# Performance work log

Measured on AMD Instinct MI355X. Metric: run time of the kernel, lower is better.

The kernel has to match this reference:

```python
import jax, jax.numpy as jnp
import numpy as np

B, T, C = 8, 2048, 1024
HEAD = 64
BLOCK = 2048  # block_size == max_size == ramp_size


def setup_inputs() -> dict:
    key = jax.random.key(0)
    kx, kq, kk, kv = jax.random.split(key, 4)
    x = jax.random.normal(kx, (B, T, C), dtype=jnp.float32)
    # torch Linear(n_embd, head_size, bias=False): store as (C, HEAD) for x @ W
    s = 1.0 / np.sqrt(C)
    Wq = jax.random.uniform(kq, (C, HEAD), dtype=jnp.float32, minval=-s, maxval=s)
    Wk = jax.random.uniform(kk, (C, HEAD), dtype=jnp.float32, minval=-s, maxval=s)
    Wv = jax.random.uniform(kv, (C, HEAD), dtype=jnp.float32, minval=-s, maxval=s)
    # adaptive_span current_val parameter, shape (1,1,1), init 0
    current_val = jnp.zeros((1, 1, 1), dtype=jnp.float32)
    return {"x": x, "Wq": Wq, "Wk": Wk, "Wv": Wv, "current_val": current_val}


def reference(x, Wq, Wk, Wv, current_val):
    Bb, Tt, Cc = x.shape
    q = x @ Wq  # (B,T,H)
    k = x @ Wk
    v = x @ Wv
    scale = 1.0 / jnp.sqrt(jnp.asarray(HEAD, dtype=x.dtype))
    scores = jnp.einsum('bth,bsh->bts', q, k) * scale  # (B,T,T)
    causal = jnp.tril(jnp.ones((Tt, Tt), dtype=bool))
    scores = jnp.where(causal, scores, -jnp.inf)
    w = jax.nn.softmax(scores, axis=-1)
    # adaptive span post-softmax mask (T == max_size here, so no slicing)
    template = jnp.linspace(1.0 - BLOCK, 0.0, BLOCK, dtype=x.dtype)  # (T,)
    span = template + current_val * BLOCK  # (1,1,T)
    span = jnp.clip(span / BLOCK + 1.0, 0.0, 1.0)
    w = w * span
    w = w / (w.sum(-1, keepdims=True) + 1e-8)
    # dropout p=0 (eval) -> identity
    out = jnp.einsum('bts,bsh->bth', w, v)  # (B,T,H)
    return out
```

## Files before the change

kernel.cpp:

```cpp
#include <hip/hip_runtime.h>
#include <hip/hip_bf16.h>

#define BSZ 8
#define T 2048
#define C 1024
#define H 64
#define M (BSZ*T)

typedef __attribute__((ext_vector_type(4))) float f32x4;
typedef __attribute__((ext_vector_type(8))) short bf16x8;
typedef __attribute__((ext_vector_type(4))) short s16x4;
typedef __attribute__((ext_vector_type(8))) short s16x8;

static __device__ __forceinline__ short f2bf(float f) {
  union { float f; unsigned u; } c; c.f = f;
  unsigned u = c.u;
  u = (u + 0x7fffu + ((u >> 16) & 1u)) >> 16;
  return (short)u;
}

static __device__ __forceinline__ float fexp2(float x) {
  float r;
  asm("v_exp_f32 %0, %1" : "=v"(r) : "v"(x));
  return r;
}

__global__ __launch_bounds__(256) void k_wt(const float* __restrict__ Wq,
                                            const float* __restrict__ Wk,
                                            const float* __restrict__ Wv,
                                            short* __restrict__ wt) {
  int idx = blockIdx.x * 256 + threadIdx.x;
  int c = idx & (C - 1);
  int n = idx >> 10;
  int w = n >> 6;
  int h = n & (H - 1);
  const float* W = (w == 0) ? Wq : (w == 1) ? Wk : Wv;
  wt[idx] = f2bf(W[c * H + h]);
}

__global__ __launch_bounds__(256) void k_qkv(const float* __restrict__ x,
                                             const short* __restrict__ wt,
                                             short* __restrict__ qb,
                                             short* __restrict__ kb,
                                             short* __restrict__ vt) {
  __shared__ short xs[2][32 * 64];
  __shared__ short wl[2][192 * 64];
  const int tid = threadIdx.x;
  const int m0 = blockIdx.x * 32;
  const int lane = tid & 63;
  const int wid = tid >> 6;
  const int g16 = lane >> 4, l16 = lane & 15;
  const int row0 = (wid & 1) * 16;
  const int nc0 = (wid >> 1) * 96;

  f32x4 acc[6];
  #pragma unroll
  for (int i = 0; i < 6; ++i) acc[i] = (f32x4){0.f, 0.f, 0.f, 0.f};

  const int xr = tid >> 4;
  const int xc4 = (tid & 15) * 4;
  const int xsw = xc4 ^ ((xr & 7) << 3);
  const int wr = tid >> 3;
  const int wc8 = (tid & 7) * 8;
  const int wsw = wc8 ^ ((wr & 7) << 3);
  const int fsw = (l16 & 7) << 3;

  float4 xA0, xA1, xB0, xB1;
  s16x8 wA0, wA1, wA2, wA3, wA4, wA5;
  s16x8 wB0, wB1, wB2, wB3, wB4, wB5;

#define QKV_LOAD(S, kc) do { \
    x##S##0 = *(const float4*)&x[(size_t)(m0 + xr) * C + (kc) + xc4]; \
    x##S##1 = *(const float4*)&x[(size_t)(m0 + xr + 16) * C + (kc) + xc4]; \
    w##S##0 = *(const s16x8*)&wt[(wr +   0) * C + (kc) + wc8]; \
    w##S##1 = *(const s16x8*)&wt[(wr +  32) * C + (kc) + wc8]; \
    w##S##2 = *(const s16x8*)&wt[(wr +  64) * C + (kc) + wc8]; \
    w##S##3 = *(const s16x8*)&wt[(wr +  96) * C + (kc) + wc8]; \
    w##S##4 = *(const s16x8*)&wt[(wr + 128) * C + (kc) + wc8]; \
    w##S##5 = *(const s16x8*)&wt[(wr + 160) * C + (kc) + wc8]; \
  } while (0)

#define QKV_STORE(S, buf) do { \
    s16x4 h0 = { f2bf((x##S##0).x), f2bf((x##S##0).y), f2bf((x##S##0).z), f2bf((x##S##0).w) }; \
    s16x4 h1 = { f2bf((x##S##1).x), f2bf((x##S##1).y), f2bf((x##S##1).z), f2bf((x##S##1).w) }; \
    *(s16x4*)&xs[buf][xr * 64 + xsw] = h0; \
    *(s16x4*)&xs[buf][(xr + 16) * 64 + xsw] = h1; \
    *(s16x8*)&wl[buf][(wr +   0) * 64 + wsw] = w##S##0; \
    *(s16x8*)&wl[buf][(wr +  32) * 64 + wsw] = w##S##1; \
    *(s16x8*)&wl[buf][(wr +  64) * 64 + wsw] = w##S##2; \
    *(s16x8*)&wl[buf][(wr +  96) * 64 + wsw] = w##S##3; \
    *(s16x8*)&wl[buf][(wr + 128) * 64 + wsw] = w##S##4; \
    *(s16x8*)&wl[buf][(wr + 160) * 64 + wsw] = w##S##5; \
  } while (0)

#define QKV_COMPUTE(buf) do { \
    _Pragma("unroll") \
    for (int ks = 0; ks < 2; ++ks) { \
      bf16x8 a = *(const bf16x8*)&xs[buf][(row0 + l16) * 64 + ((ks * 32 + g16 * 8) ^ fsw)]; \
      _Pragma("unroll") \
      for (int nt = 0; nt < 6; ++nt) { \
        bf16x8 bfr = *(const bf16x8*)&wl[buf][(nc0 + nt * 16 + l16) * 64 + ((ks * 32 + g16 * 8) ^ fsw)]; \
        acc[nt] = __builtin_amdgcn_mfma_f32_16x16x32_bf16(a, bfr, acc[nt], 0, 0, 0); \
      } \
    } \
  } while (0)

  QKV_LOAD(A, 0);
  QKV_STORE(A, 0);
  QKV_LOAD(B, 64);
  __syncthreads();

  #pragma unroll 1
  for (int ii = 0; ii < 8; ++ii) {
    if (ii < 7) QKV_LOAD(A, (2 * ii + 2) * 64);
    QKV_STORE(B, 1);
    QKV_COMPUTE(0);
    __syncthreads();
    if (ii < 7) {
      QKV_LOAD(B, (2 * ii + 3) * 64);
      QKV_STORE(A, 0);
    }
    QKV_COMPUTE(1);
    if (ii < 7) __syncthreads();
  }
#undef QKV_LOAD
#undef QKV_STORE
#undef QKV_COMPUTE

  const int r0 = row0 + g16 * 4;
  #pragma unroll
  for (int nt = 0; nt < 6; ++nt) {
    const int nglob = nc0 + nt * 16;
    const int which = nglob >> 6;
    const int col = (nglob & 63) + l16;
    #pragma unroll
    for (int j = 0; j < 4; ++j) {
      const int tg = m0 + r0 + j;
      const short val = f2bf(acc[nt][j]);
      if (which == 0)      qb[tg * H + col] = val;
      else if (which == 1) kb[tg * H + col] = val;
      else {
        const int b = tg >> 11, tl = tg & (T - 1);
        vt[((b << 6) + col) * T + tl] = val;
      }
    }
  }
}

__global__ __launch_bounds__(512, 2) void k_attn(const short* __restrict__ qb,
                                                 const short* __restrict__ kb,
                                                 const short* __restrict__ vt,
                                                 const float* __restrict__ cvp,
                                                 float* __restrict__ out) {
  __shared__ float Ow[8][16][68];
  __shared__ float mw[8][16];
  __shared__ float Lw[8][16];
  const int pid = blockIdx.x;
  const int b = pid & 7;
  const int pr = pid >> 3;
  const int q0A = pr << 4, q0B = (127 - pr) << 4;
  const int nitA = (q0A + 47) >> 5;
  const int nitB = (q0B + 47) >> 5;
  const int NT = nitA + nitB;
  int wA = (8 * nitA + (NT >> 1)) / NT;
  wA = wA < 1 ? 1 : (wA > 7 ? 7 : wA);

  const int tid = threadIdx.x;
  const int wid = tid >> 6;
  const int lane = tid & 63;
  const int g16 = lane >> 4, l16 = lane & 15;
  const float cv = cvp[0];
  const float SCL = 0.125f * 1.44269504f;

  const bool onA = (wid < wA);
  const int q0 = onA ? q0A : q0B;
  const int nitW = onA ? nitA : nitB;
  const int nwt = onA ? wA : 8 - wA;
  const int wg = onA ? wid : wid - wA;
  const int npw = (nitW + nwt - 1) / nwt;
  const int lo = wg * npw;
  const int hi = (lo + npw < nitW) ? lo + npw : nitW;

  const short* qp = qb + ((size_t)(b << 11) + q0 + l16) * H + g16 * 8;
  bf16x8 qf0 = *(const bf16x8*)qp;
  bf16x8 qf1 = *(const bf16x8*)(qp + 32);
  const int qg = q0 + l16;

  const int gsel = (g16 & 1) << 5;
  const int addrA = (gsel + l16) << 2;
  const int addrB = (gsel + 16 + l16) << 2;
  const bool ghi = (g16 >= 2);

  float m = -3e38f, L = 0.f;
  f32x4 O[4];
  #pragma unroll
  for (int t4 = 0; t4 < 4; ++t4) O[t4] = (f32x4){0.f, 0.f, 0.f, 0.f};

  if (lo < hi) {
    const short* kp = kb + ((size_t)(b << 11) + lo * 32 + l16) * H + g16 * 8;
    const short* vp = vt + ((size_t)(b << 6) + l16) * T + lo * 32 + g16 * 8;
    bf16x8 k00 = *(const bf16x8*)kp;
    bf16x8 k01 = *(const bf16x8*)(kp + 32);
    bf16x8 k02 = *(const bf16x8*)(kp + 16 * H);
    bf16x8 k03 = *(const bf16x8*)(kp + 16 * H + 32);
    kp += 32 * H;
    bf16x8 k10 = k00, k11 = k01, k12 = k02, k13 = k03;
    if (lo + 1 < hi) {
      k10 = *(const bf16x8*)kp;
      k11 = *(const bf16x8*)(kp + 32);
      k12 = *(const bf16x8*)(kp + 16 * H);
      k13 = *(const bf16x8*)(kp + 16 * H + 32);
      kp += 32 * H;
    }

    #pragma unroll 1
    for (int it = lo; it < hi; it += 2) {
      const bool has2 = (it + 1 < hi);
      bf16x8 vA0 = *(const bf16x8*)vp;
      bf16x8 vA1 = *(const bf16x8*)(vp + 16 * T);
      bf16x8 vA2 = *(const bf16x8*)(vp + 32 * T);
      bf16x8 vA3 = *(const bf16x8*)(vp + 48 * T);
      bf16x8 vB0 = vA0, vB1 = vA1, vB2 = vA2, vB3 = vA3;
      if (has2) {
        vB0 = *(const bf16x8*)(vp + 32);
        vB1 = *(const bf16x8*)(vp + 16 * T + 32);
        vB2 = *(const bf16x8*)(vp + 32 * T + 32);
        vB3 = *(const bf16x8*)(vp + 48 * T + 32);
      }
      bf16x8 n00, n01, n02, n03, n10, n11, n12, n13;
      const bool pf0 = (it + 2 < hi), pf1 = (it + 3 < hi);
      if (pf0) {
        n00 = *(const bf16x8*)kp;
        n01 = *(const bf16x8*)(kp + 32);
        n02 = *(const bf16x8*)(kp + 16 * H);
        n03 = *(const bf16x8*)(kp + 16 * H + 32);
        kp += 32 * H;
      }
      if (pf1) {
        n10 = *(const bf16x8*)kp;
        n11 = *(const bf16x8*)(kp + 32);
        n12 = *(const bf16x8*)(kp + 16 * H);
        n13 = *(const bf16x8*)(kp + 16 * H + 32);
        kp += 32 * H;
      }

      f32x4 sA0 = {0.f,0.f,0.f,0.f}, sA1 = {0.f,0.f,0.f,0.f};
      f32x4 sB0 = {0.f,0.f,0.f,0.f}, sB1 = {0.f,0.f,0.f,0.f};
      sA0 = __builtin_amdgcn_mfma_f32_16x16x32_bf16(k00, qf0, sA0, 0, 0, 0);
      sB0 = __builtin_amdgcn_mfma_f32_16x16x32_bf16(k10, qf0, sB0, 0, 0, 0);
      sA1 = __builtin_amdgcn_mfma_f32_16x16x32_bf16(k02, qf0, sA1, 0, 0, 0);
      sB1 = __builtin_amdgcn_mfma_f32_16x16x32_bf16(k12, qf0, sB1, 0, 0, 0);
      sA0 = __builtin_amdgcn_mfma_f32_16x16x32_bf16(k01, qf1, sA0, 0, 0, 0);
      sB0 = __builtin_amdgcn_mfma_f32_16x16x32_bf16(k11, qf1, sB0, 0, 0, 0);
      sA1 = __builtin_amdgcn_mfma_f32_16x16x32_bf16(k03, qf1, sA1, 0, 0, 0);
      sB1 = __builtin_amdgcn_mfma_f32_16x16x32_bf16(k13, qf1, sB1, 0, 0, 0);

      const int kv0A = it << 5, kv0B = kv0A + 32;
      const int kvbA = kv0A + g16 * 4, kvbB = kv0B + g16 * 4;
      const bool diagA = (kv0A + 31 > q0);
      float svA[8], svB[8];
      if (diagA) {
        #pragma unroll
        for (int r = 0; r < 8; ++r) {
          const int kvg = kvbA + ((r >> 2) << 4) + (r & 3);
          const float s = ((r < 4) ? sA0[r] : sA1[r - 4]) * SCL;
          svA[r] = (kvg <= qg) ? s : -1e30f;
        }
      } else {
        #pragma unroll
        for (int r = 0; r < 8; ++r)
          svA[r] = ((r < 4) ? sA0[r] : sA1[r - 4]) * SCL;
      }
      if (has2) {
        const bool diagB = (kv0B + 31 > q0);
        if (diagB) {
          #pragma unroll
          for (int r = 0; r < 8; ++r) {
            const int kvg = kvbB + ((r >> 2) << 4) + (r & 3);
            const float s = ((r < 4) ? sB0[r] : sB1[r - 4]) * SCL;
            svB[r] = (kvg <= qg) ? s : -1e30f;
          }
        } else {
          #pragma unroll
          for (int r = 0; r < 8; ++r)
            svB[r] = ((r < 4) ? sB0[r] : sB1[r - 4]) * SCL;
        }
      } else {
        #pragma unroll
        for (int r = 0; r < 8; ++r) svB[r] = -1e30f;
      }

      float pmax = -3e38f;
      #pragma unroll
      for (int r = 0; r < 8; ++r) pmax = fmaxf(pmax, fmaxf(svA[r], svB[r]));
      if (!__all(pmax <= m + 7.f)) {
        float v = pmax;
        v = fmaxf(v, __shfl_xor(v, 16, 64));
        v = fmaxf(v, __shfl_xor(v, 32, 64));
        const float mn = fmaxf(m, v);
        const float al = fexp2(m - mn);
        m = mn;
        L *= al;
        #pragma unroll
        for (int t4 = 0; t4 < 4; ++t4) O[t4] *= al;
      }

      float pA[8], pB[8];
      #pragma unroll
      for (int r = 0; r < 8; ++r) {
        const int kvgA = kvbA + ((r >> 2) << 4) + (r & 3);
        const float spA = fminf(fmaxf((float)(kvgA + 1) * (1.f / 2048.f) + cv, 0.f), 1.f);
        pA[r] = fexp2(svA[r] - m) * spA;
        const float spB = fminf(fmaxf((float)(kvgA + 33) * (1.f / 2048.f) + cv, 0.f), 1.f);
        pB[r] = fexp2(svB[r] - m) * spB;
      }
      if (diagA) {
        #pragma unroll
        for (int r = 0; r < 8; ++r) {
          const int kvg = kvbA + ((r >> 2) << 4) + (r & 3);
          pA[r] = (kvg <= qg) ? pA[r] : 0.f;
          pB[r] = (kvg + 32 <= qg) ? pB[r] : 0.f;
        }
      } else if (kv0B + 31 > q0) {
        #pragma unroll
        for (int r = 0; r < 8; ++r) {
          const int kvg = kvbB + ((r >> 2) << 4) + (r & 3);
          pB[r] = (kvg <= qg) ? pB[r] : 0.f;
        }
      }
      L += ((pA[0] + pA[1]) + (pA[2] + pA[3])) + ((pA[4] + pA[5]) + (pA[6] + pA[7]))
         + ((pB[0] + pB[1]) + (pB[2] + pB[3])) + ((pB[4] + pB[5]) + (pB[6] + pB[7]));

      union { float f; unsigned u; } a0, a1;
      unsigned dA0, dA1, dA2, dA3, dB0, dB1, dB2, dB3;
      a0.f = pA[0]; a1.f = pA[1]; dA0 = (a0.u >> 16) | (a1.u & 0xffff0000u);
      a0.f = pA[2]; a1.f = pA[3]; dA1 = (a0.u >> 16) | (a1.u & 0xffff0000u);
      a0.f = pA[4]; a1.f = pA[5]; dA2 = (a0.u >> 16) | (a1.u & 0xffff0000u);
      a0.f = pA[6]; a1.f = pA[7]; dA3 = (a0.u >> 16) | (a1.u & 0xffff0000u);
      a0.f = pB[0]; a1.f = pB[1]; dB0 = (a0.u >> 16) | (a1.u & 0xffff0000u);
      a0.f = pB[2]; a1.f = pB[3]; dB1 = (a0.u >> 16) | (a1.u & 0xffff0000u);
      a0.f = pB[4]; a1.f = pB[5]; dB2 = (a0.u >> 16) | (a1.u & 0xffff0000u);
      a0.f = pB[6]; a1.f = pB[7]; dB3 = (a0.u >> 16) | (a1.u & 0xffff0000u);
      const int Alo0 = __builtin_amdgcn_ds_bpermute(addrA, (int)dA0);
      const int Alo1 = __builtin_amdgcn_ds_bpermute(addrA, (int)dA1);
      const int Alo2 = __builtin_amdgcn_ds_bpermute(addrB, (int)dA0);
      const int Alo3 = __builtin_amdgcn_ds_bpermute(addrB, (int)dA1);
      const int Ahi0 = __builtin_amdgcn_ds_bpermute(addrA, (int)dA2);
      const int Ahi1 = __builtin_amdgcn_ds_bpermute(addrA, (int)dA3);
      const int Ahi2 = __builtin_amdgcn_ds_bpermute(addrB, (int)dA2);
      const int Ahi3 = __builtin_amdgcn_ds_bpermute(addrB, (int)dA3);
      const int Blo0 = __builtin_amdgcn_ds_bpermute(addrA, (int)dB0);
      const int Blo1 = __builtin_amdgcn_ds_bpermute(addrA, (int)dB1);
      const int Blo2 = __builtin_amdgcn_ds_bpermute(addrB, (int)dB0);
      const int Blo3 = __builtin_amdgcn_ds_bpermute(addrB, (int)dB1);
      const int Bhi0 = __builtin_amdgcn_ds_bpermute(addrA, (int)dB2);
      const int Bhi1 = __builtin_amdgcn_ds_bpermute(addrA, (int)dB3);
      const int Bhi2 = __builtin_amdgcn_ds_bpermute(addrB, (int)dB2);
      const int Bhi3 = __builtin_amdgcn_ds_bpermute(addrB, (int)dB3);
      union { int w[4]; bf16x8 v8; } puA, puB;
      puA.w[0] = ghi ? Ahi0 : Alo0;
      puA.w[1] = ghi ? Ahi1 : Alo1;
      puA.w[2] = ghi ? Ahi2 : Alo2;
      puA.w[3] = ghi ? Ahi3 : Alo3;
      puB.w[0] = ghi ? Bhi0 : Blo0;
      puB.w[1] = ghi ? Bhi1 : Blo1;
      puB.w[2] = ghi ? Bhi2 : Blo2;
      puB.w[3] = ghi ? Bhi3 : Blo3;
      const bf16x8 paA = puA.v8;
      const bf16x8 paB = puB.v8;

      O[0] = __builtin_amdgcn_mfma_f32_16x16x32_bf16(vA0, paA, O[0], 0, 0, 0);
      O[1] = __builtin_amdgcn_mfma_f32_16x16x32_bf16(vA1, paA, O[1], 0, 0, 0);
      O[2] = __builtin_amdgcn_mfma_f32_16x16x32_bf16(vA2, paA, O[2], 0, 0, 0);
      O[3] = __builtin_amdgcn_mfma_f32_16x16x32_bf16(vA3, paA, O[3], 0, 0, 0);
      if (has2) {
        O[0] = __builtin_amdgcn_mfma_f32_16x16x32_bf16(vB0, paB, O[0], 0, 0, 0);
        O[1] = __builtin_amdgcn_mfma_f32_16x16x32_bf16(vB1, paB, O[1], 0, 0, 0);
        O[2] = __builtin_amdgcn_mfma_f32_16x16x32_bf16(vB2, paB, O[2], 0, 0, 0);
        O[3] = __builtin_amdgcn_mfma_f32_16x16x32_bf16(vB3, paB, O[3], 0, 0, 0);
      }

      if (pf0) { k00 = n00; k01 = n01; k02 = n02; k03 = n03; }
      if (pf1) { k10 = n10; k11 = n11; k12 = n12; k13 = n13; }
      vp += 64;
    }
  }

  float Lr = L;
  Lr += __shfl_xor(Lr, 16, 64);
  Lr += __shfl_xor(Lr, 32, 64);
  if (g16 == 0) { mw[wid][l16] = m; Lw[wid][l16] = Lr; }
  #pragma unroll
  for (int t4 = 0; t4 < 4; ++t4)
    *(f32x4*)&Ow[wid][l16][t4 * 16 + g16 * 4] = O[t4];
  __syncthreads();

  {
    const int r32 = tid >> 4;
    const int c4 = (tid & 15) << 2;
    const bool rowA = (r32 < 16);
    const int r = rowA ? r32 : r32 - 16;
    const int w0 = rowA ? 0 : wA;
    const int w1 = rowA ? wA : 8;
    const int q0r = rowA ? q0A : q0B;
    float Mx = -3e38f;
    for (int w = w0; w < w1; ++w) Mx = fmaxf(Mx, mw[w][r]);
    float Ls = 0.f;
    f32x4 o = (f32x4){0.f, 0.f, 0.f, 0.f};
    for (int w = w0; w < w1; ++w) {
      const float fw = fexp2(mw[w][r] - Mx);
      Ls += Lw[w][r] * fw;
      f32x4 ow = *(const f32x4*)&Ow[w][r][c4];
      o += ow * fw;
    }
    o *= 1.f / (Ls + 1e-30f);
    *(f32x4*)&out[(size_t)((b << 11) + q0r + r) * H + c4] = o;
  }
}

extern "C" void kernel_launch(void* const* d_in, const int* in_sizes, int n_in,
                              void* d_out, int out_size, void* d_ws, size_t ws_size,
                              hipStream_t stream) {
  const float* x  = (const float*)d_in[0];
  const float* Wq = (const float*)d_in[1];
  const float* Wk = (const float*)d_in[2];
  const float* Wv = (const float*)d_in[3];
  const float* cv = (const float*)d_in[4];
  float* out = (float*)d_out;

  char* ws = (char*)d_ws;
  short* qb = (short*)(ws);
  short* kb = (short*)(ws + (size_t)M * H * 2);
  short* vt = (short*)(ws + (size_t)2 * M * H * 2);
  short* wt = (short*)(ws + (size_t)3 * M * H * 2);

  hipLaunchKernelGGL(k_wt, dim3(3 * H * C / 256), dim3(256), 0, stream, Wq, Wk, Wv, wt);
  hipLaunchKernelGGL(k_qkv, dim3(M / 32), dim3(256), 0, stream, x, wt, qb, kb, vt);
  hipLaunchKernelGGL(k_attn, dim3(BSZ * T / 32), dim3(512), 0, stream, qb, kb, vt, cv, out);
}
```

Measured before the change: 66.31 us.

## Load QKV projection MFMA fragments directly from global, dropping LDS staging

The QKV projection kernel no longer stages x and the weights through shared memory with barriers. Each wave now loads its own MFMA operand fragments straight from global memory into registers, converts x to bf16 on the fly, and software-pipelines the loads against the MFMAs. This removes LDS traffic and __syncthreads, and launch bounds now request two blocks per CU. The cost is redundant global loads across waves, which must be absorbed by the cache, plus more register pressure.

```diff
diff --git a/kernel.cpp b/kernel.cpp
--- a/kernel.cpp
+++ b/kernel.cpp
@@ -38,13 +38,11 @@
   wt[idx] = f2bf(W[c * H + h]);
 }
 
-__global__ __launch_bounds__(256) void k_qkv(const float* __restrict__ x,
-                                             const short* __restrict__ wt,
-                                             short* __restrict__ qb,
-                                             short* __restrict__ kb,
-                                             short* __restrict__ vt) {
-  __shared__ short xs[2][32 * 64];
-  __shared__ short wl[2][192 * 64];
+__global__ __launch_bounds__(256, 2) void k_qkv(const float* __restrict__ x,
+                                                const short* __restrict__ wt,
+                                                short* __restrict__ qb,
+                                                short* __restrict__ kb,
+                                                short* __restrict__ vt) {
   const int tid = threadIdx.x;
   const int m0 = blockIdx.x * 32;
   const int lane = tid & 63;
@@ -57,75 +55,64 @@
   #pragma unroll
   for (int i = 0; i < 6; ++i) acc[i] = (f32x4){0.f, 0.f, 0.f, 0.f};
 
-  const int xr = tid >> 4;
-  const int xc4 = (tid & 15) * 4;
-  const int xsw = xc4 ^ ((xr & 7) << 3);
-  const int wr = tid >> 3;
-  const int wc8 = (tid & 7) * 8;
-  const int wsw = wc8 ^ ((wr & 7) << 3);
-  const int fsw = (l16 & 7) << 3;
-
-  float4 xA0, xA1, xB0, xB1;
-  s16x8 wA0, wA1, wA2, wA3, wA4, wA5;
-  s16x8 wB0, wB1, wB2, wB3, wB4, wB5;
-
-#define QKV_LOAD(S, kc) do { \
-    x##S##0 = *(const float4*)&x[(size_t)(m0 + xr) * C + (kc) + xc4]; \
-    x##S##1 = *(const float4*)&x[(size_t)(m0 + xr + 16) * C + (kc) + xc4]; \
-    w##S##0 = *(const s16x8*)&wt[(wr +   0) * C + (kc) + wc8]; \
-    w##S##1 = *(const s16x8*)&wt[(wr +  32) * C + (kc) + wc8]; \
-    w##S##2 = *(const s16x8*)&wt[(wr +  64) * C + (kc) + wc8]; \
-    w##S##3 = *(const s16x8*)&wt[(wr +  96) * C + (kc) + wc8]; \
-    w##S##4 = *(const s16x8*)&wt[(wr + 128) * C + (kc) + wc8]; \
-    w##S##5 = *(const s16x8*)&wt[(wr + 160) * C + (kc) + wc8]; \
+  float4 xA0, xA1, xA2, xA3, xB0, xB1, xB2, xB3;
+  s16x8 w00, w01, w02, w03, w04, w05;
+  s16x8 w10, w11, w12, w13, w14, w15;
+
+  const float* xrow = &x[(size_t)(m0 + row0 + l16) * C + g16 * 8];
+  const short* wrow = &wt[(size_t)(nc0 + l16) * C + g16 * 8];
+
+#define XL(S, kc) do { \
+    const float* xb = xrow + (kc); \
+    x##S##0 = *(const float4*)(xb); \
+    x##S##1 = *(const float4*)(xb + 4); \
+    x##S##2 = *(const float4*)(xb + 32); \
+    x##S##3 = *(const float4*)(xb + 36); \
   } while (0)
 
-#define QKV_STORE(S, buf) do { \
-    s16x4 h0 = { f2bf((x##S##0).x), f2bf((x##S##0).y), f2bf((x##S##0).z), f2bf((x##S##0).w) }; \
-    s16x4 h1 = { f2bf((x##S##1).x), f2bf((x##S##1).y), f2bf((x##S##1).z), f2bf((x##S##1).w) }; \
-    *(s16x4*)&xs[buf][xr * 64 + xsw] = h0; \
-    *(s16x4*)&xs[buf][(xr + 16) * 64 + xsw] = h1; \
-    *(s16x8*)&wl[buf][(wr +   0) * 64 + wsw] = w##S##0; \
-    *(s16x8*)&wl[buf][(wr +  32) * 64 + wsw] = w##S##1; \
-    *(s16x8*)&wl[buf][(wr +  64) * 64 + wsw] = w##S##2; \
-    *(s16x8*)&wl[buf][(wr +  96) * 64 + wsw] = w##S##3; \
-    *(s16x8*)&wl[buf][(wr + 128) * 64 + wsw] = w##S##4; \
-    *(s16x8*)&wl[buf][(wr + 160) * 64 + wsw] = w##S##5; \
+#define WLH(P, kc, ks) do { \
+    const short* wb = wrow + (kc) + (ks) * 32; \
+    P##0 = *(const s16x8*)(wb); \
+    P##1 = *(const s16x8*)(wb + 16 * C); \
+    P##2 = *(const s16x8*)(wb + 32 * C); \
+    P##3 = *(const s16x8*)(wb + 48 * C); \
+    P##4 = *(const s16x8*)(wb + 64 * C); \
+    P##5 = *(const s16x8*)(wb + 80 * C); \
   } while (0)
 
-#define QKV_COMPUTE(buf) do { \
-    _Pragma("unroll") \
-    for (int ks = 0; ks < 2; ++ks) { \
-      bf16x8 a = *(const bf16x8*)&xs[buf][(row0 + l16) * 64 + ((ks * 32 + g16 * 8) ^ fsw)]; \
-      _Pragma("unroll") \
-      for (int nt = 0; nt < 6; ++nt) { \
-        bf16x8 bfr = *(const bf16x8*)&wl[buf][(nc0 + nt * 16 + l16) * 64 + ((ks * 32 + g16 * 8) ^ fsw)]; \
-        acc[nt] = __builtin_amdgcn_mfma_f32_16x16x32_bf16(a, bfr, acc[nt], 0, 0, 0); \
-      } \
-    } \
+#define MFMA_HALF(P, S, i0, i1) do { \
+    bf16x8 a = { f2bf((x##S##i0).x), f2bf((x##S##i0).y), f2bf((x##S##i0).z), f2bf((x##S##i0).w), \
+                 f2bf((x##S##i1).x), f2bf((x##S##i1).y), f2bf((x##S##i1).z), f2bf((x##S##i1).w) }; \
+    acc[0] = __builtin_amdgcn_mfma_f32_16x16x32_bf16(a, P##0, acc[0], 0, 0, 0); \
+    acc[1] = __builtin_amdgcn_mfma_f32_16x16x32_bf16(a, P##1, acc[1], 0, 0, 0); \
+    acc[2] = __builtin_amdgcn_mfma_f32_16x16x32_bf16(a, P##2, acc[2], 0, 0, 0); \
+    acc[3] = __builtin_amdgcn_mfma_f32_16x16x32_bf16(a, P##3, acc[3], 0, 0, 0); \
+    acc[4] = __builtin_amdgcn_mfma_f32_16x16x32_bf16(a, P##4, acc[4], 0, 0, 0); \
+    acc[5] = __builtin_amdgcn_mfma_f32_16x16x32_bf16(a, P##5, acc[5], 0, 0, 0); \
   } while (0)
 
-  QKV_LOAD(A, 0);
-  QKV_STORE(A, 0);
-  QKV_LOAD(B, 64);
-  __syncthreads();
+  XL(A, 0);
+  WLH(w0, 0, 0);
+  WLH(w1, 0, 1);
 
   #pragma unroll 1
   for (int ii = 0; ii < 8; ++ii) {
-    if (ii < 7) QKV_LOAD(A, (2 * ii + 2) * 64);
-    QKV_STORE(B, 1);
-    QKV_COMPUTE(0);
-    __syncthreads();
-    if (ii < 7) {
-      QKV_LOAD(B, (2 * ii + 3) * 64);
-      QKV_STORE(A, 0);
-    }
-    QKV_COMPUTE(1);
-    if (ii < 7) __syncthreads();
+    const int kc1 = (2 * ii + 1) * 64;
+    const int kc2 = (2 * ii + 2) * 64;
+    XL(B, kc1);
+    MFMA_HALF(w0, A, 0, 1);
+    WLH(w0, kc1, 0);
+    MFMA_HALF(w1, A, 2, 3);
+    WLH(w1, kc1, 1);
+    if (ii < 7) XL(A, kc2);
+    MFMA_HALF(w0, B, 0, 1);
+    if (ii < 7) WLH(w0, kc2, 0);
+    MFMA_HALF(w1, B, 2, 3);
+    if (ii < 7) WLH(w1, kc2, 1);
   }
-#undef QKV_LOAD
-#undef QKV_STORE
-#undef QKV_COMPUTE
+#undef XL
+#undef WLH
+#undef MFMA_HALF
 
   const int r0 = row0 + g16 * 4;
   #pragma unroll
```

Result: slower. 104.9 us (+58.2%).
